# Performance work log

Measured on AMD Instinct MI355X. Metric: run time of the kernel, lower is better.

The kernel has to match this reference:

```python
import jax, jax.numpy as jnp
import numpy as np

N = 50000
E = 800000
D_IN = 128
D_HID = 256
D_OUT = 128
BN_EPS = 1e-5


def setup_inputs() -> dict:
    key = jax.random.key(0)
    ks = jax.random.split(key, 12)
    v = jax.random.normal(ks[0], (N, D_IN), dtype=jnp.float32)
    edge_rows = jax.random.randint(ks[1], (E,), 0, N)
    edge_cols = jax.random.randint(ks[2], (E,), 0, N)
    edge_vals = jax.random.uniform(ks[3], (E,), dtype=jnp.float32)
    s1 = 1.0 / np.sqrt(D_IN)
    s2 = 1.0 / np.sqrt(D_HID)
    w1 = jax.random.uniform(ks[4], (D_IN, D_HID), minval=-s1, maxval=s1, dtype=jnp.float32)
    b1 = jax.random.uniform(ks[5], (D_HID,), minval=-s1, maxval=s1, dtype=jnp.float32)
    g1 = jnp.ones((D_HID,), dtype=jnp.float32)
    be1 = jnp.zeros((D_HID,), dtype=jnp.float32)
    w2 = jax.random.uniform(ks[6], (D_HID, D_OUT), minval=-s2, maxval=s2, dtype=jnp.float32)
    b2 = jax.random.uniform(ks[7], (D_OUT,), minval=-s2, maxval=s2, dtype=jnp.float32)
    g2 = jnp.ones((D_OUT,), dtype=jnp.float32)
    be2 = jnp.zeros((D_OUT,), dtype=jnp.float32)
    epsilon = jnp.zeros((1, 1), dtype=jnp.float32)  # nn.Parameter([[0.0]])
    return {"v": v, "edge_rows": edge_rows, "edge_cols": edge_cols,
            "edge_vals": edge_vals, "w1": w1, "b1": b1, "g1": g1, "be1": be1,
            "w2": w2, "b2": b2, "g2": g2, "be2": be2, "epsilon": epsilon}


def _batch_norm_relu(x, gamma, beta):
    # training-mode BatchNorm1d: batch stats over node axis, biased variance
    mean = jnp.mean(x, axis=0)
    var = jnp.var(x, axis=0)
    xhat = (x - mean) * jax.lax.rsqrt(var + BN_EPS)
    return jax.nn.relu(xhat * gamma + beta)


def reference(v, edge_rows, edge_cols, edge_vals, w1, b1, g1, be1, w2, b2, g2, be2, epsilon):
    # v_aggregate = sparse.mm(a, v): agg[r] += a[r,c] * v[c]
    msgs = edge_vals[:, None] * v[edge_cols]           # [E, D_IN]
    v_agg = jax.ops.segment_sum(msgs, edge_rows, num_segments=N)
    v_agg = v_agg + epsilon * v                         # epsilon residual ([[eps]] broadcasts)
    h = _batch_norm_relu(v_agg @ w1 + b1, g1, be1)      # Linear + BN + ReLU
    out = _batch_norm_relu(h @ w2 + b2, g2, be2)        # Linear + BN + ReLU
    return out
```

## Files before the change

kernel.cpp:

```cpp
#include <hip/hip_runtime.h>

#define D_IN 128
#define D_HID 256
#define D_OUT 128
#define BN_EPS 1e-5f

__global__ __launch_bounds__(256) void edge_hist(
    const int* __restrict__ rows, int* __restrict__ cnt, int E)
{
    int e = blockIdx.x * 256 + threadIdx.x;
    if (e < E) atomicAdd(&cnt[rows[e]], 1);
}

__global__ __launch_bounds__(256) void chunk_sums(
    const int* __restrict__ cnt, int* __restrict__ bsum, int N)
{
    __shared__ int red[256];
    const int t = threadIdx.x;
    const int i = blockIdx.x * 256 + t;
    red[t] = (i < N) ? cnt[i] : 0;
    __syncthreads();
#pragma unroll
    for (int off = 128; off > 0; off >>= 1) {
        if (t < off) red[t] += red[t + off];
        __syncthreads();
    }
    if (t == 0) bsum[blockIdx.x] = red[0];
}

__global__ __launch_bounds__(256) void scan_chunks(
    const int* __restrict__ bsum, int* __restrict__ coff, int NB)
{
    __shared__ int s[256];
    const int t = threadIdx.x;
    int c = (t < NB) ? bsum[t] : 0;
    s[t] = c;
    __syncthreads();
#pragma unroll
    for (int off = 1; off < 256; off <<= 1) {
        int x = (t >= off) ? s[t - off] : 0;
        __syncthreads();
        s[t] += x;
        __syncthreads();
    }
    coff[t] = s[t] - c;
}

__global__ __launch_bounds__(256) void scan_write(
    const int* __restrict__ cnt, const int* __restrict__ coff,
    int* __restrict__ rowstart, int* __restrict__ cursor, int N)
{
    __shared__ int s[256];
    const int t = threadIdx.x;
    const int i = blockIdx.x * 256 + t;
    int c = (i < N) ? cnt[i] : 0;
    s[t] = c;
    __syncthreads();
#pragma unroll
    for (int off = 1; off < 256; off <<= 1) {
        int x = (t >= off) ? s[t - off] : 0;
        __syncthreads();
        s[t] += x;
        __syncthreads();
    }
    int pos = coff[blockIdx.x] + s[t] - c;
    if (i < N) {
        rowstart[i] = pos;
        cursor[i] = pos;
    } else if (i == N) {
        rowstart[N] = pos;
    }
}

__global__ __launch_bounds__(256) void edge_scatter(
    const int* __restrict__ rows, const int* __restrict__ cols,
    const float* __restrict__ vals, int* __restrict__ cursor,
    float2* __restrict__ ecv, int E)
{
    int e = blockIdx.x * 256 + threadIdx.x;
    if (e >= E) return;
    int r = rows[e];
    int pos = atomicAdd(&cursor[r], 1);
    ecv[pos] = make_float2(__int_as_float(cols[e]), vals[e]);
}

__global__ __launch_bounds__(256) void spmm_rows(
    const float* __restrict__ v, const int* __restrict__ rowstart,
    const float2* __restrict__ ecv, const float* __restrict__ epsp,
    float* __restrict__ x, int N)
{
    int wid = (blockIdx.x * 256 + threadIdx.x) >> 6;
    if (wid >= N) return;
    const int lane = threadIdx.x & 63;
    const int half = lane >> 5;
    const int l32 = lane & 31;
    const int s = rowstart[wid], e = rowstart[wid + 1];
    float4 acc = make_float4(0.f, 0.f, 0.f, 0.f);

    for (int base = s; base < e; base += 64) {
        int n = min(64, e - base);
        float2 ev = make_float2(0.f, 0.f);
        if (base + lane < e) ev = ecv[base + lane];
        int mycol = __float_as_int(ev.x);
        int pairs = (n + 1) >> 1;
        for (int k = 0; k < pairs; ++k) {
            int idx = 2 * k + half;
            int col = __shfl(mycol, idx);
            float val = __shfl(ev.y, idx);
            const float4 vv = *reinterpret_cast<const float4*>(
                v + (size_t)col * D_IN + l32 * 4);
            acc.x = fmaf(val, vv.x, acc.x);
            acc.y = fmaf(val, vv.y, acc.y);
            acc.z = fmaf(val, vv.z, acc.z);
            acc.w = fmaf(val, vv.w, acc.w);
        }
    }
    acc.x += __shfl_down(acc.x, 32);
    acc.y += __shfl_down(acc.y, 32);
    acc.z += __shfl_down(acc.z, 32);
    acc.w += __shfl_down(acc.w, 32);
    if (half == 0) {
        const float eps = *epsp;
        const float4 vs = *reinterpret_cast<const float4*>(
            v + (size_t)wid * D_IN + l32 * 4);
        float4 o;
        o.x = fmaf(eps, vs.x, acc.x);
        o.y = fmaf(eps, vs.y, acc.y);
        o.z = fmaf(eps, vs.z, acc.z);
        o.w = fmaf(eps, vs.w, acc.w);
        *reinterpret_cast<float4*>(x + (size_t)wid * D_IN + l32 * 4) = o;
    }
}

__global__ __launch_bounds__(256) void gemm1(
    const float* __restrict__ x, const float* __restrict__ w1,
    float* __restrict__ y1, float* __restrict__ sum, float* __restrict__ sq,
    int M)
{
    __shared__ __align__(16) float As[32][68];
    __shared__ __align__(16) float Bs[32][64];
    const int tid = threadIdx.x;
    const int bm = blockIdx.x * 64;
    const int bn = blockIdx.y * 64;
    const int lr = tid >> 3, lc = (tid & 7) << 2;
    const int br = tid >> 4, bc = (tid & 15) << 2;
    const int ty = tid >> 4, tx = tid & 15;
    float acc[4][4] = {};

    for (int kk = 0; kk < D_IN; kk += 32) {
#pragma unroll
        for (int h = 0; h < 2; ++h) {
            int row = bm + lr + h * 32;
            float4 a = make_float4(0.f, 0.f, 0.f, 0.f);
            if (row < M)
                a = *reinterpret_cast<const float4*>(x + (size_t)row * D_IN + kk + lc);
            As[lc + 0][lr + h * 32] = a.x;
            As[lc + 1][lr + h * 32] = a.y;
            As[lc + 2][lr + h * 32] = a.z;
            As[lc + 3][lr + h * 32] = a.w;
        }
#pragma unroll
        for (int h = 0; h < 2; ++h) {
            int krow = kk + br + h * 16;
            *reinterpret_cast<float4*>(&Bs[br + h * 16][bc]) =
                *reinterpret_cast<const float4*>(w1 + (size_t)krow * D_HID + bn + bc);
        }
        __syncthreads();
#pragma unroll
        for (int k = 0; k < 32; ++k) {
            float4 a4 = *reinterpret_cast<float4*>(&As[k][ty * 4]);
            float4 b4 = *reinterpret_cast<float4*>(&Bs[k][tx * 4]);
            float af[4] = {a4.x, a4.y, a4.z, a4.w};
            float bf[4] = {b4.x, b4.y, b4.z, b4.w};
#pragma unroll
            for (int i = 0; i < 4; ++i)
#pragma unroll
                for (int j = 0; j < 4; ++j)
                    acc[i][j] = fmaf(af[i], bf[j], acc[i][j]);
        }
        __syncthreads();
    }
#pragma unroll
    for (int i = 0; i < 4; ++i) {
        int row = bm + ty * 4 + i;
        if (row < M) {
            float4 o = make_float4(acc[i][0], acc[i][1], acc[i][2], acc[i][3]);
            *reinterpret_cast<float4*>(y1 + (size_t)row * D_HID + bn + tx * 4) = o;
        }
    }
    float* red = &As[0][0];
#pragma unroll
    for (int j = 0; j < 4; ++j) {
        float s = acc[0][j] + acc[1][j] + acc[2][j] + acc[3][j];
        float q = acc[0][j] * acc[0][j] + acc[1][j] * acc[1][j]
                + acc[2][j] * acc[2][j] + acc[3][j] * acc[3][j];
        red[ty * 64 + tx * 4 + j]        = s;
        red[1024 + ty * 64 + tx * 4 + j] = q;
    }
    __syncthreads();
    if (tid < 64) {
        float s = 0.f, q = 0.f;
#pragma unroll
        for (int t = 0; t < 16; ++t) {
            s += red[t * 64 + tid];
            q += red[1024 + t * 64 + tid];
        }
        atomicAdd(&sum[bn + tid], s);
        atomicAdd(&sq[bn + tid], q);
    }
}

__global__ __launch_bounds__(256) void gemm2(
    const float* __restrict__ y1, const float2* __restrict__ f1,
    const float* __restrict__ w2, float* __restrict__ y2,
    float* __restrict__ sum, float* __restrict__ sq, int M)
{
    __shared__ __align__(16) float As[32][68];
    __shared__ __align__(16) float Bs[32][64];
    const int tid = threadIdx.x;
    const int bm = blockIdx.x * 64;
    const int bn = blockIdx.y * 64;
    const int lr = tid >> 3, lc = (tid & 7) << 2;
    const int br = tid >> 4, bc = (tid & 15) << 2;
    const int ty = tid >> 4, tx = tid & 15;
    float acc[4][4] = {};

    for (int kk = 0; kk < D_HID; kk += 32) {
#pragma unroll
        for (int h = 0; h < 2; ++h) {
            int row = bm + lr + h * 32;
            float4 a = make_float4(0.f, 0.f, 0.f, 0.f);
            if (row < M) {
                const float4 xx = *reinterpret_cast<const float4*>(y1 + (size_t)row * D_HID + kk + lc);
                float2 fa = f1[kk + lc + 0];
                float2 fb = f1[kk + lc + 1];
                float2 fc = f1[kk + lc + 2];
                float2 fd = f1[kk + lc + 3];
                a.x = fmaxf(fmaf(xx.x, fa.x, fa.y), 0.f);
                a.y = fmaxf(fmaf(xx.y, fb.x, fb.y), 0.f);
                a.z = fmaxf(fmaf(xx.z, fc.x, fc.y), 0.f);
                a.w = fmaxf(fmaf(xx.w, fd.x, fd.y), 0.f);
            }
            As[lc + 0][lr + h * 32] = a.x;
            As[lc + 1][lr + h * 32] = a.y;
            As[lc + 2][lr + h * 32] = a.z;
            As[lc + 3][lr + h * 32] = a.w;
        }
#pragma unroll
        for (int h = 0; h < 2; ++h) {
            int krow = kk + br + h * 16;
            *reinterpret_cast<float4*>(&Bs[br + h * 16][bc]) =
                *reinterpret_cast<const float4*>(w2 + (size_t)krow * D_OUT + bn + bc);
        }
        __syncthreads();
#pragma unroll
        for (int k = 0; k < 32; ++k) {
            float4 a4 = *reinterpret_cast<float4*>(&As[k][ty * 4]);
            float4 b4 = *reinterpret_cast<float4*>(&Bs[k][tx * 4]);
            float af[4] = {a4.x, a4.y, a4.z, a4.w};
            float bf[4] = {b4.x, b4.y, b4.z, b4.w};
#pragma unroll
            for (int i = 0; i < 4; ++i)
#pragma unroll
                for (int j = 0; j < 4; ++j)
                    acc[i][j] = fmaf(af[i], bf[j], acc[i][j]);
        }
        __syncthreads();
    }
#pragma unroll
    for (int i = 0; i < 4; ++i) {
        int row = bm + ty * 4 + i;
        if (row < M) {
            float4 o = make_float4(acc[i][0], acc[i][1], acc[i][2], acc[i][3]);
            *reinterpret_cast<float4*>(y2 + (size_t)row * D_OUT + bn + tx * 4) = o;
        }
    }
    float* red = &As[0][0];
#pragma unroll
    for (int j = 0; j < 4; ++j) {
        float s = acc[0][j] + acc[1][j] + acc[2][j] + acc[3][j];
        float q = acc[0][j] * acc[0][j] + acc[1][j] * acc[1][j]
                + acc[2][j] * acc[2][j] + acc[3][j] * acc[3][j];
        red[ty * 64 + tx * 4 + j]        = s;
        red[1024 + ty * 64 + tx * 4 + j] = q;
    }
    __syncthreads();
    if (tid < 64) {
        float s = 0.f, q = 0.f;
#pragma unroll
        for (int t = 0; t < 16; ++t) {
            s += red[t * 64 + tid];
            q += red[1024 + t * 64 + tid];
        }
        atomicAdd(&sum[bn + tid], s);
        atomicAdd(&sq[bn + tid], q);
    }
}

__global__ void bnfactors(const float* __restrict__ sum, const float* __restrict__ sq,
                          const float* __restrict__ g, const float* __restrict__ be,
                          float2* __restrict__ f, int C, int M)
{
    int c = threadIdx.x;
    if (c < C) {
        float inv = 1.f / (float)M;
        float mean = sum[c] * inv;
        float var = fmaxf(sq[c] * inv - mean * mean, 0.f);
        float s = g[c] * rsqrtf(var + BN_EPS);
        f[c] = make_float2(s, be[c] - mean * s);
    }
}

__global__ __launch_bounds__(256) void bnrelu_out(
    const float* __restrict__ y2, const float2* __restrict__ f2,
    float* __restrict__ out, int total4)
{
    int i = blockIdx.x * 256 + threadIdx.x;
    if (i >= total4) return;
    float4 x = reinterpret_cast<const float4*>(y2)[i];
    int c = (i & (D_OUT / 4 - 1)) << 2;
    float2 fa = f2[c + 0];
    float2 fb = f2[c + 1];
    float2 fc = f2[c + 2];
    float2 fd = f2[c + 3];
    float4 o;
    o.x = fmaxf(fmaf(x.x, fa.x, fa.y), 0.f);
    o.y = fmaxf(fmaf(x.y, fb.x, fb.y), 0.f);
    o.z = fmaxf(fmaf(x.z, fc.x, fc.y), 0.f);
    o.w = fmaxf(fmaf(x.w, fd.x, fd.y), 0.f);
    reinterpret_cast<float4*>(out)[i] = o;
}

extern "C" void kernel_launch(void* const* d_in, const int* in_sizes, int n_in,
                              void* d_out, int out_size, void* d_ws, size_t ws_size,
                              hipStream_t stream)
{
    const float* v     = (const float*)d_in[0];
    const int*   erows = (const int*)d_in[1];
    const int*   ecols = (const int*)d_in[2];
    const float* evals = (const float*)d_in[3];
    const float* w1    = (const float*)d_in[4];
    const float* g1    = (const float*)d_in[6];
    const float* be1   = (const float*)d_in[7];
    const float* w2    = (const float*)d_in[8];
    const float* g2    = (const float*)d_in[10];
    const float* be2   = (const float*)d_in[11];
    const float* eps   = (const float*)d_in[12];

    const int M = in_sizes[0] / D_IN;
    const int E = in_sizes[3];
    const int NB = (M + 255) / 256;

    float* ws   = (float*)d_ws;
    float* x    = ws;
    float* y1   = x + (size_t)M * D_IN;
    int*  rowstart = (int*)(y1 + (size_t)M * D_HID);
    int*  cursor   = rowstart + M + 2;
    int*  cnthist  = cursor + M;
    int*  bsum     = cnthist + M;
    int*  coff     = bsum + 256;
    size_t ecv_ofs = ((size_t)(coff + 256 - (int*)ws) + 1) & ~(size_t)1;
    float2* ecv = (float2*)((float*)ws + ecv_ofs);
    float* st   = (float*)(ecv + E);
    float* sum1 = st;
    float* sq1  = sum1 + D_HID;
    float* sum2 = sq1 + D_HID;
    float* sq2  = sum2 + D_OUT;
    float2* f1  = (float2*)(sq2 + D_OUT);
    float2* f2  = f1 + D_HID;
    float* y2   = x;
    float* outp = (float*)d_out;

    hipMemsetAsync(cnthist, 0, (size_t)M * sizeof(int), stream);
    hipMemsetAsync(st, 0, (size_t)(2 * D_HID + 2 * D_OUT) * sizeof(float), stream);

    edge_hist<<<(E + 255) / 256, 256, 0, stream>>>(erows, cnthist, E);
    chunk_sums<<<NB, 256, 0, stream>>>(cnthist, bsum, M);
    scan_chunks<<<1, 256, 0, stream>>>(bsum, coff, NB);
    scan_write<<<NB, 256, 0, stream>>>(cnthist, coff, rowstart, cursor, M);
    edge_scatter<<<(E + 255) / 256, 256, 0, stream>>>(erows, ecols, evals, cursor, ecv, E);
    spmm_rows<<<(M * 64 + 255) / 256, 256, 0, stream>>>(v, rowstart, ecv, eps, x, M);

    dim3 grid1((M + 63) / 64, D_HID / 64);
    gemm1<<<grid1, 256, 0, stream>>>(x, w1, y1, sum1, sq1, M);
    bnfactors<<<1, D_HID, 0, stream>>>(sum1, sq1, g1, be1, f1, D_HID, M);

    dim3 grid2((M + 63) / 64, D_OUT / 64);
    gemm2<<<grid2, 256, 0, stream>>>(y1, f1, w2, y2, sum2, sq2, M);
    bnfactors<<<1, D_OUT, 0, stream>>>(sum2, sq2, g2, be2, f2, D_OUT, M);

    bnrelu_out<<<(M * D_OUT / 4 + 255) / 256, 256, 0, stream>>>(y2, f2, outp, M * D_OUT / 4);
}
```

Measured before the change: 398.6 us.

## Replace FP32 SIMT GEMMs with bf16 MFMA GEMMs and bf16 intermediates

```diff
diff --git a/kernel.cpp b/kernel.cpp
--- a/kernel.cpp
+++ b/kernel.cpp
@@ -4,6 +4,34 @@
 #define D_HID 256
 #define D_OUT 128
 #define BN_EPS 1e-5f
+
+typedef unsigned short u16;
+typedef unsigned int u32;
+typedef __attribute__((ext_vector_type(8))) short bf16x8;
+typedef __attribute__((ext_vector_type(4))) float f32x4;
+
+__device__ __forceinline__ u16 f2b(float f) {
+    u32 u = __float_as_uint(f);
+    return (u16)((u + 0x7FFFu + ((u >> 16) & 1u)) >> 16);
+}
+__device__ __forceinline__ float b2f(u16 h) {
+    return __uint_as_float(((u32)h) << 16);
+}
+
+__global__ __launch_bounds__(256) void cvt_w(
+    const float* __restrict__ w1, const float* __restrict__ w2,
+    u16* __restrict__ w1t, u16* __restrict__ w2t)
+{
+    int i = blockIdx.x * 256 + threadIdx.x;
+    if (i < 32768) {
+        int n = i >> 7, k = i & 127;
+        w1t[i] = f2b(w1[k * 256 + n]);
+    } else {
+        int j = i - 32768;
+        int n = j >> 8, k = j & 255;
+        w2t[j] = f2b(w2[k * 128 + n]);
+    }
+}
 
 __global__ __launch_bounds__(256) void edge_hist(
     const int* __restrict__ rows, int* __restrict__ cnt, int E)
@@ -87,7 +115,7 @@
 __global__ __launch_bounds__(256) void spmm_rows(
     const float* __restrict__ v, const int* __restrict__ rowstart,
     const float2* __restrict__ ecv, const float* __restrict__ epsp,
-    float* __restrict__ x, int N)
+    u16* __restrict__ x, int N)
 {
     int wid = (blockIdx.x * 256 + threadIdx.x) >> 6;
     if (wid >= N) return;
@@ -123,177 +151,123 @@
         const float eps = *epsp;
         const float4 vs = *reinterpret_cast<const float4*>(
             v + (size_t)wid * D_IN + l32 * 4);
-        float4 o;
-        o.x = fmaf(eps, vs.x, acc.x);
-        o.y = fmaf(eps, vs.y, acc.y);
-        o.z = fmaf(eps, vs.z, acc.z);
-        o.w = fmaf(eps, vs.w, acc.w);
-        *reinterpret_cast<float4*>(x + (size_t)wid * D_IN + l32 * 4) = o;
-    }
-}
-
-__global__ __launch_bounds__(256) void gemm1(
-    const float* __restrict__ x, const float* __restrict__ w1,
-    float* __restrict__ y1, float* __restrict__ sum, float* __restrict__ sq,
-    int M)
-{
-    __shared__ __align__(16) float As[32][68];
-    __shared__ __align__(16) float Bs[32][64];
+        u32 a0 = (u32)f2b(fmaf(eps, vs.x, acc.x)) |
+                 ((u32)f2b(fmaf(eps, vs.y, acc.y)) << 16);
+        u32 a1 = (u32)f2b(fmaf(eps, vs.z, acc.z)) |
+                 ((u32)f2b(fmaf(eps, vs.w, acc.w)) << 16);
+        *reinterpret_cast<uint2*>(x + (size_t)wid * D_IN + l32 * 4) =
+            make_uint2(a0, a1);
+    }
+}
+
+template <int KT, int NSTR, bool BNA>
+__global__ __launch_bounds__(256) void gemm_mf(
+    const u16* __restrict__ A, const u16* __restrict__ Bt,
+    const float2* __restrict__ fA, u16* __restrict__ C,
+    float* __restrict__ sum, float* __restrict__ sq, int M)
+{
+    __shared__ u16 As[64 * 128];
+    __shared__ u16 Bs[128 * 128];
+    __shared__ float2 fs[256];
+
     const int tid = threadIdx.x;
     const int bm = blockIdx.x * 64;
-    const int bn = blockIdx.y * 64;
-    const int lr = tid >> 3, lc = (tid & 7) << 2;
-    const int br = tid >> 4, bc = (tid & 15) << 2;
-    const int ty = tid >> 4, tx = tid & 15;
-    float acc[4][4] = {};
-
-    for (int kk = 0; kk < D_IN; kk += 32) {
-#pragma unroll
-        for (int h = 0; h < 2; ++h) {
-            int row = bm + lr + h * 32;
-            float4 a = make_float4(0.f, 0.f, 0.f, 0.f);
-            if (row < M)
-                a = *reinterpret_cast<const float4*>(x + (size_t)row * D_IN + kk + lc);
-            As[lc + 0][lr + h * 32] = a.x;
-            As[lc + 1][lr + h * 32] = a.y;
-            As[lc + 2][lr + h * 32] = a.z;
-            As[lc + 3][lr + h * 32] = a.w;
-        }
-#pragma unroll
-        for (int h = 0; h < 2; ++h) {
-            int krow = kk + br + h * 16;
-            *reinterpret_cast<float4*>(&Bs[br + h * 16][bc]) =
-                *reinterpret_cast<const float4*>(w1 + (size_t)krow * D_HID + bn + bc);
-        }
-        __syncthreads();
-#pragma unroll
-        for (int k = 0; k < 32; ++k) {
-            float4 a4 = *reinterpret_cast<float4*>(&As[k][ty * 4]);
-            float4 b4 = *reinterpret_cast<float4*>(&Bs[k][tx * 4]);
-            float af[4] = {a4.x, a4.y, a4.z, a4.w};
-            float bf[4] = {b4.x, b4.y, b4.z, b4.w};
-#pragma unroll
-            for (int i = 0; i < 4; ++i)
-#pragma unroll
-                for (int j = 0; j < 4; ++j)
-                    acc[i][j] = fmaf(af[i], bf[j], acc[i][j]);
-        }
-        __syncthreads();
-    }
+    const int bn0 = blockIdx.y * 128;
+    const int l = tid & 63;
+    const int wm = (tid >> 6) * 16;
+    char* AsB = reinterpret_cast<char*>(As);
+    char* BsB = reinterpret_cast<char*>(Bs);
+
+    if (BNA) fs[tid] = fA[tid];
+
+    f32x4 acc[8];
+#pragma unroll
+    for (int t = 0; t < 8; ++t) acc[t] = (f32x4){0.f, 0.f, 0.f, 0.f};
+
+    for (int kk = 0; kk < KT; kk += 128) {
+        __syncthreads();
+#pragma unroll
+        for (int i = 0; i < 4; ++i) {
+            int c = tid + i * 256;
+            int row = c >> 4, slot = c & 15;
+            uint4 val = make_uint4(0u, 0u, 0u, 0u);
+            if (bm + row < M)
+                val = *reinterpret_cast<const uint4*>(
+                    A + (size_t)(bm + row) * KT + kk + slot * 8);
+            if (BNA) {
+                u16* hp = reinterpret_cast<u16*>(&val);
+#pragma unroll
+                for (int j = 0; j < 8; ++j) {
+                    float2 f = fs[kk + slot * 8 + j];
+                    hp[j] = f2b(fmaxf(fmaf(b2f(hp[j]), f.x, f.y), 0.f));
+                }
+            }
+            *reinterpret_cast<uint4*>(
+                AsB + ((row * 256 + slot * 16) ^ ((row & 7) << 4))) = val;
+        }
+#pragma unroll
+        for (int i = 0; i < 8; ++i) {
+            int c = tid + i * 256;
+            int n = c >> 4, slot = c & 15;
+            uint4 val = *reinterpret_cast<const uint4*>(
+                Bt + (size_t)(bn0 + n) * KT + kk + slot * 8);
+            *reinterpret_cast<uint4*>(
+                BsB + ((n * 256 + slot * 16) ^ ((n & 7) << 4))) = val;
+        }
+        __syncthreads();
+#pragma unroll
+        for (int s = 0; s < 4; ++s) {
+            int ka = (s * 32 + (l >> 4) * 8) * 2;
+            int arow = wm + (l & 15);
+            bf16x8 af = *reinterpret_cast<bf16x8*>(
+                AsB + ((arow * 256 + ka) ^ ((l & 7) << 4)));
+#pragma unroll
+            for (int t = 0; t < 8; ++t) {
+                int brow = t * 16 + (l & 15);
+                bf16x8 bfr = *reinterpret_cast<bf16x8*>(
+                    BsB + ((brow * 256 + ka) ^ ((l & 7) << 4)));
+                acc[t] = __builtin_amdgcn_mfma_f32_16x16x32_bf16(
+                    af, bfr, acc[t], 0, 0, 0);
+            }
+        }
+    }
+
+#pragma unroll
+    for (int t = 0; t < 8; ++t) {
+        float s = acc[t][0] + acc[t][1] + acc[t][2] + acc[t][3];
+        float q = acc[t][0] * acc[t][0] + acc[t][1] * acc[t][1]
+                + acc[t][2] * acc[t][2] + acc[t][3] * acc[t][3];
+        s += __shfl_down(s, 32);  q += __shfl_down(q, 32);
+        s += __shfl_down(s, 16);  q += __shfl_down(q, 16);
+        if ((l >> 4) == 0) {
+            atomicAdd(&sum[bn0 + t * 16 + l], s);
+            atomicAdd(&sq[bn0 + t * 16 + l], q);
+        }
+    }
+
+    __syncthreads();
+#pragma unroll
+    for (int t = 0; t < 8; ++t) {
+#pragma unroll
+        for (int r = 0; r < 4; ++r) {
+            int row = wm + (l >> 4) * 4 + r;
+            int col = t * 16 + (l & 15);
+            *reinterpret_cast<u16*>(
+                AsB + ((row * 256 + col * 2) ^ ((row & 7) << 4))) =
+                f2b(acc[t][r]);
+        }
+    }
+    __syncthreads();
 #pragma unroll
     for (int i = 0; i < 4; ++i) {
-        int row = bm + ty * 4 + i;
-        if (row < M) {
-            float4 o = make_float4(acc[i][0], acc[i][1], acc[i][2], acc[i][3]);
-            *reinterpret_cast<float4*>(y1 + (size_t)row * D_HID + bn + tx * 4) = o;
-        }
-    }
-    float* red = &As[0][0];
-#pragma unroll
-    for (int j = 0; j < 4; ++j) {
-        float s = acc[0][j] + acc[1][j] + acc[2][j] + acc[3][j];
-        float q = acc[0][j] * acc[0][j] + acc[1][j] * acc[1][j]
-                + acc[2][j] * acc[2][j] + acc[3][j] * acc[3][j];
-        red[ty * 64 + tx * 4 + j]        = s;
-        red[1024 + ty * 64 + tx * 4 + j] = q;
-    }
-    __syncthreads();
-    if (tid < 64) {
-        float s = 0.f, q = 0.f;
-#pragma unroll
-        for (int t = 0; t < 16; ++t) {
-            s += red[t * 64 + tid];
-            q += red[1024 + t * 64 + tid];
-        }
-        atomicAdd(&sum[bn + tid], s);
-        atomicAdd(&sq[bn + tid], q);
-    }
-}
-
-__global__ __launch_bounds__(256) void gemm2(
-    const float* __restrict__ y1, const float2* __restrict__ f1,
-    const float* __restrict__ w2, float* __restrict__ y2,
-    float* __restrict__ sum, float* __restrict__ sq, int M)
-{
-    __shared__ __align__(16) float As[32][68];
-    __shared__ __align__(16) float Bs[32][64];
-    const int tid = threadIdx.x;
-    const int bm = blockIdx.x * 64;
-    const int bn = blockIdx.y * 64;
-    const int lr = tid >> 3, lc = (tid & 7) << 2;
-    const int br = tid >> 4, bc = (tid & 15) << 2;
-    const int ty = tid >> 4, tx = tid & 15;
-    float acc[4][4] = {};
-
-    for (int kk = 0; kk < D_HID; kk += 32) {
-#pragma unroll
-        for (int h = 0; h < 2; ++h) {
-            int row = bm + lr + h * 32;
-            float4 a = make_float4(0.f, 0.f, 0.f, 0.f);
-            if (row < M) {
-                const float4 xx = *reinterpret_cast<const float4*>(y1 + (size_t)row * D_HID + kk + lc);
-                float2 fa = f1[kk + lc + 0];
-                float2 fb = f1[kk + lc + 1];
-                float2 fc = f1[kk + lc + 2];
-                float2 fd = f1[kk + lc + 3];
-                a.x = fmaxf(fmaf(xx.x, fa.x, fa.y), 0.f);
-                a.y = fmaxf(fmaf(xx.y, fb.x, fb.y), 0.f);
-                a.z = fmaxf(fmaf(xx.z, fc.x, fc.y), 0.f);
-                a.w = fmaxf(fmaf(xx.w, fd.x, fd.y), 0.f);
-            }
-            As[lc + 0][lr + h * 32] = a.x;
-            As[lc + 1][lr + h * 32] = a.y;
-            As[lc + 2][lr + h * 32] = a.z;
-            As[lc + 3][lr + h * 32] = a.w;
-        }
-#pragma unroll
-        for (int h = 0; h < 2; ++h) {
-            int krow = kk + br + h * 16;
-            *reinterpret_cast<float4*>(&Bs[br + h * 16][bc]) =
-                *reinterpret_cast<const float4*>(w2 + (size_t)krow * D_OUT + bn + bc);
-        }
-        __syncthreads();
-#pragma unroll
-        for (int k = 0; k < 32; ++k) {
-            float4 a4 = *reinterpret_cast<float4*>(&As[k][ty * 4]);
-            float4 b4 = *reinterpret_cast<float4*>(&Bs[k][tx * 4]);
-            float af[4] = {a4.x, a4.y, a4.z, a4.w};
-            float bf[4] = {b4.x, b4.y, b4.z, b4.w};
-#pragma unroll
-            for (int i = 0; i < 4; ++i)
-#pragma unroll
-                for (int j = 0; j < 4; ++j)
-                    acc[i][j] = fmaf(af[i], bf[j], acc[i][j]);
-        }
-        __syncthreads();
-    }
-#pragma unroll
-    for (int i = 0; i < 4; ++i) {
-        int row = bm + ty * 4 + i;
-        if (row < M) {
-            float4 o = make_float4(acc[i][0], acc[i][1], acc[i][2], acc[i][3]);
-            *reinterpret_cast<float4*>(y2 + (size_t)row * D_OUT + bn + tx * 4) = o;
-        }
-    }
-    float* red = &As[0][0];
-#pragma unroll
-    for (int j = 0; j < 4; ++j) {
-        float s = acc[0][j] + acc[1][j] + acc[2][j] + acc[3][j];
-        float q = acc[0][j] * acc[0][j] + acc[1][j] * acc[1][j]
-                + acc[2][j] * acc[2][j] + acc[3][j] * acc[3][j];
-        red[ty * 64 + tx * 4 + j]        = s;
-        red[1024 + ty * 64 + tx * 4 + j] = q;
-    }
-    __syncthreads();
-    if (tid < 64) {
-        float s = 0.f, q = 0.f;
-#pragma unroll
-        for (int t = 0; t < 16; ++t) {
-            s += red[t * 64 + tid];
-            q += red[1024 + t * 64 + tid];
-        }
-        atomicAdd(&sum[bn + tid], s);
-        atomicAdd(&sq[bn + tid], q);
+        int c = tid + i * 256;
+        int row = c >> 4, slot = c & 15;
+        if (bm + row < M) {
+            uint4 val = *reinterpret_cast<uint4*>(
+                AsB + ((row * 256 + slot * 16) ^ ((row & 7) << 4)));
+            *reinterpret_cast<uint4*>(
+                C + (size_t)(bm + row) * NSTR + bn0 + slot * 8) = val;
+        }
     }
 }
 
@@ -312,23 +286,24 @@
 }
 
 __global__ __launch_bounds__(256) void bnrelu_out(
-    const float* __restrict__ y2, const float2* __restrict__ f2,
-    float* __restrict__ out, int total4)
+    const u16* __restrict__ y2, const float2* __restrict__ f2,
+    float* __restrict__ out, int total8)
 {
     int i = blockIdx.x * 256 + threadIdx.x;
-    if (i >= total4) return;
-    float4 x = reinterpret_cast<const float4*>(y2)[i];
-    int c = (i & (D_OUT / 4 - 1)) << 2;
-    float2 fa = f2[c + 0];
-    float2 fb = f2[c + 1];
-    float2 fc = f2[c + 2];
-    float2 fd = f2[c + 3];
-    float4 o;
-    o.x = fmaxf(fmaf(x.x, fa.x, fa.y), 0.f);
-    o.y = fmaxf(fmaf(x.y, fb.x, fb.y), 0.f);
-    o.z = fmaxf(fmaf(x.z, fc.x, fc.y), 0.f);
-    o.w = fmaxf(fmaf(x.w, fd.x, fd.y), 0.f);
-    reinterpret_cast<float4*>(out)[i] = o;
+    if (i >= total8) return;
+    uint4 val = *reinterpret_cast<const uint4*>(y2 + (size_t)i * 8);
+    const u16* hp = reinterpret_cast<const u16*>(&val);
+    int c = (i & 15) * 8;
+    float r[8];
+#pragma unroll
+    for (int j = 0; j < 8; ++j) {
+        float2 f = f2[c + j];
+        r[j] = fmaxf(fmaf(b2f(hp[j]), f.x, f.y), 0.f);
+    }
+    *reinterpret_cast<float4*>(out + (size_t)i * 8) =
+        make_float4(r[0], r[1], r[2], r[3]);
+    *reinterpret_cast<float4*>(out + (size_t)i * 8 + 4) =
+        make_float4(r[4], r[5], r[6], r[7]);
 }
 
 extern "C" void kernel_launch(void* const* d_in, const int* in_sizes, int n_in,
@@ -351,16 +326,17 @@
     const int E = in_sizes[3];
     const int NB = (M + 255) / 256;
 
-    float* ws   = (float*)d_ws;
-    float* x    = ws;
-    float* y1   = x + (size_t)M * D_IN;
-    int*  rowstart = (int*)(y1 + (size_t)M * D_HID);
-    int*  cursor   = rowstart + M + 2;
-    int*  cnthist  = cursor + M;
-    int*  bsum     = cnthist + M;
-    int*  coff     = bsum + 256;
-    size_t ecv_ofs = ((size_t)(coff + 256 - (int*)ws) + 1) & ~(size_t)1;
-    float2* ecv = (float2*)((float*)ws + ecv_ofs);
+    u16* xb  = (u16*)d_ws;
+    u16* y1b = xb + (size_t)M * D_IN;
+    u16* w1t = y1b + (size_t)M * D_HID;
+    u16* w2t = w1t + 32768;
+    int* rowstart = (int*)(w2t + 32768);
+    int* cursor   = rowstart + M + 2;
+    int* cnthist  = cursor + M;
+    int* bsum     = cnthist + M;
+    int* coff     = bsum + 256;
+    size_t ecv_ofs = ((size_t)(coff + 256 - (int*)d_ws) + 1) & ~(size_t)1;
+    float2* ecv = (float2*)((float*)d_ws + ecv_ofs);
     float* st   = (float*)(ecv + E);
     float* sum1 = st;
     float* sq1  = sum1 + D_HID;
@@ -368,26 +344,30 @@
     float* sq2  = sum2 + D_OUT;
     float2* f1  = (float2*)(sq2 + D_OUT);
     float2* f2  = f1 + D_HID;
-    float* y2   = x;
+    u16* y2b    = xb;
     float* outp = (float*)d_out;
 
     hipMemsetAsync(cnthist, 0, (size_t)M * sizeof(int), stream);
     hipMemsetAsync(st, 0, (size_t)(2 * D_HID + 2 * D_OUT) * sizeof(float), stream);
 
+    cvt_w<<<256, 256, 0, stream>>>(w1, w2, w1t, w2t);
     edge_hist<<<(E + 255) / 256, 256, 0, stream>>>(erows, cnthist, E);
     chunk_sums<<<NB, 256, 0, stream>>>(cnthist, bsum, M);
     scan_chunks<<<1, 256, 0, stream>>>(bsum, coff, NB);
     scan_write<<<NB, 256, 0, stream>>>(cnthist, coff, rowstart, cursor, M);
     edge_scatter<<<(E + 255) / 256, 256, 0, stream>>>(erows, ecols, evals, cursor, ecv, E);
-    spmm_rows<<<(M * 64 + 255) / 256, 256, 0, stream>>>(v, rowstart, ecv, eps, x, M);
-
-    dim3 grid1((M + 63) / 64, D_HID / 64);
-    gemm1<<<grid1, 256, 0, stream>>>(x, w1, y1, sum1, sq1, M);
+    spmm_rows<<<(M * 64 + 255) / 256, 256, 0, stream>>>(v, rowstart, ecv, eps, xb, M);
+
+    dim3 grid1((M + 63) / 64, 2);
+    gemm_mf<128, 256, false><<<grid1, 256, 0, stream>>>(
+        xb, w1t, nullptr, y1b, sum1, sq1, M);
     bnfactors<<<1, D_HID, 0, stream>>>(sum1, sq1, g1, be1, f1, D_HID, M);
 
-    dim3 grid2((M + 63) / 64, D_OUT / 64);
-    gemm2<<<grid2, 256, 0, stream>>>(y1, f1, w2, y2, sum2, sq2, M);
+    dim3 grid2((M + 63) / 64, 1);
+    gemm_mf<256, 128, true><<<grid2, 256, 0, stream>>>(
+        y1b, w2t, f1, y2b, sum2, sq2, M);
     bnfactors<<<1, D_OUT, 0, stream>>>(sum2, sq2, g2, be2, f2, D_OUT, M);
 
-    bnrelu_out<<<(M * D_OUT / 4 + 255) / 256, 256, 0, stream>>>(y2, f2, outp, M * D_OUT / 4);
-}
+    bnrelu_out<<<(M * D_OUT / 8 + 255) / 256, 256, 0, stream>>>(
+        y2b, f2, outp, M * D_OUT / 8);
+}
```

New measurement: 670.0 us. 1.68x slower.
